# Kernel optimization log

Hardware: AMD Instinct MI355X
Metric: run time of the kernel (lower is better)

## Reference

```python
import jax, jax.numpy as jnp
import numpy as np

STRIDES = (8.0, 16.0, 32.0)


def _decode_level(feat, W, b, stride, level):
    # feat: [bs, C, ny, nx]; W: [85, C]; b: [85]
    bs, _, ny, nx = feat.shape
    # 1x1 conv == channel contraction; output laid out as [bs, ny, nx, 85]
    p = jnp.einsum('bchw,oc->bhwo', feat, W) + b
    y = jax.nn.sigmoid(p)
    xv = jnp.arange(nx, dtype=y.dtype)            # broadcasts over last spatial dim
    yv = jnp.arange(ny, dtype=y.dtype)[:, None]   # broadcasts over row dim
    power = jnp.asarray(2.0 ** level, dtype=y.dtype)
    d = (y[..., :4] * 2.0) ** 2 * power           # dx1, dy1, dx2, dy2
    x1 = (xv + 1.0 - d[..., 0]) * stride
    y1 = (yv + 1.0 - d[..., 1]) * stride
    x2 = (xv + d[..., 2]) * stride
    y2 = (yv + d[..., 3]) * stride
    # xyxy -> xywh
    box = jnp.stack([(x1 + x2) * 0.5, (y1 + y2) * 0.5, x2 - x1, y2 - y1], axis=-1)
    out = jnp.concatenate([box, y[..., 4:]], axis=-1)  # [bs, ny, nx, 85]
    return out.reshape(bs, ny * nx, out.shape[-1])


def setup_inputs() -> dict:
    key = jax.random.key(0)
    ks = jax.random.split(key, 9)
    f32 = jnp.float32
    return {
        'x0': jax.random.normal(ks[0], (16, 256, 80, 80), dtype=f32),
        'x1': jax.random.normal(ks[1], (16, 512, 40, 40), dtype=f32),
        'x2': jax.random.normal(ks[2], (16, 1024, 20, 20), dtype=f32),
        'W0': jax.random.normal(ks[3], (85, 256), dtype=f32) * 0.05,
        'b0': jax.random.normal(ks[4], (85,), dtype=f32) * 0.05,
        'W1': jax.random.normal(ks[5], (85, 512), dtype=f32) * 0.05,
        'b1': jax.random.normal(ks[6], (85,), dtype=f32) * 0.05,
        'W2': jax.random.normal(ks[7], (85, 1024), dtype=f32) * 0.05,
        'b2': jax.random.normal(ks[8], (85,), dtype=f32) * 0.05,
    }


def reference(x0, x1, x2, W0, b0, W1, b1, W2, b2):
    feats = (x0, x1, x2)
    Ws = (W0, W1, W2)
    bs_ = (b0, b1, b2)
    z = [_decode_level(feats[i], Ws[i], bs_[i], STRIDES[i], i) for i in range(3)]
    return jnp.concatenate(z, axis=1)  # [bs, 8400, 85]
```

## Files before the change

### kernel.cpp

```cpp
#include <hip/hip_runtime.h>
#include <cstdint>


typedef __attribute__((ext_vector_type(8))) short bf16x8;
typedef __attribute__((ext_vector_type(4))) float f32x4;

constexpr int KS0 = 8, KS1 = 16, KS2 = 32;
constexpr int F0 = 6 * KS0, F1 = 6 * KS1, F2 = 6 * KS2;
constexpr int FOFF0 = 0, FOFF1 = F0, FOFF2 = F0 + F1;
constexpr int NFRAG = F0 + F1 + F2;
constexpr size_t BIAS_OFF = 0;
constexpr size_t BPK_OFF  = 1152;
constexpr size_t WS_NEED  = BPK_OFF + (size_t)NFRAG * 64 * 16;

__device__ __forceinline__ unsigned short f2bf(float f) {
    union { float f; unsigned u; } v; v.f = f;
    unsigned r = v.u + 0x7FFF + ((v.u >> 16) & 1);
    return (unsigned short)(r >> 16);
}

__global__ __launch_bounds__(256) void prep_pack(
    const float* __restrict__ W0, const float* __restrict__ W1,
    const float* __restrict__ W2,
    const float* __restrict__ b0, const float* __restrict__ b1,
    const float* __restrict__ b2,
    unsigned char* __restrict__ ws)
{
    int t = blockIdx.x * 256 + threadIdx.x;
    if (t < 288) {
        int lvl = t / 96, o = t % 96;
        const float* bp = (lvl == 0) ? b0 : (lvl == 1) ? b1 : b2;
        ((float*)(ws + BIAS_OFF))[t] = (o < 85) ? bp[o] : 0.0f;
    }
    if (t >= NFRAG * 64) return;
    int frag = t >> 6, l = t & 63;
    int C; const float* W; int f;
    if (frag < FOFF1)      { C = 256;  W = W0; f = frag;         }
    else if (frag < FOFF2) { C = 512;  W = W1; f = frag - FOFF1; }
    else                   { C = 1024; W = W2; f = frag - FOFF2; }
    int ks = f / 6, n = f % 6;
    int o  = n * 16 + (l & 15);
    int c0 = ks * 32 + (l >> 4) * 8;
    bf16x8 r;
#pragma unroll
    for (int e = 0; e < 8; ++e)
        r[e] = (o < 85) ? (short)f2bf(W[(size_t)o * C + c0 + e]) : (short)0;
    ((bf16x8*)(ws + BPK_OFF))[frag * 64 + l] = r;
}

template <int C, int HW, int NX, int LEVEL, int AOFF, int KSTEPS, int FOFF>
__device__ __forceinline__ void mfma_level(
    const float* __restrict__ feat, const unsigned char* __restrict__ ws,
    float* __restrict__ out, int blk, uint4* __restrict__ Bsm )
{
    const int tid = threadIdx.x;
    const int w   = tid >> 6;
    const int l   = tid & 63;
    const int col = l & 15;
    const int kg  = l >> 4;
    const bool lo_half = (tid < 128);

    const int p0  = blk * 64 + w * 16;
    const int b   = p0 / HW;
    const int hw0 = p0 - b * HW;
    const float* fb = feat + (size_t)b * C * HW + hw0;
    const float* pA = fb + col + (size_t)(kg * 8) * HW;

    const float* bias = (const float*)(ws + BIAS_OFF) + LEVEL * 96;
    const uint4* bsrc = (const uint4*)(ws + BPK_OFF) + (size_t)FOFF * 64;

    f32x4 acc[6];
#pragma unroll
    for (int n = 0; n < 6; ++n) {
        float bv = bias[n * 16 + col];
        f32x4 z = { bv, bv, bv, bv };
        acc[n] = z;
    }

    uint4* buf0 = Bsm;
    uint4* buf1 = Bsm + 384;

    {
        const uint4* s = bsrc;
        buf0[tid] = s[tid];
        if (lo_half) buf0[256 + tid] = s[256 + tid];
    }
    float flA0[8], flA1[8];
#pragma unroll
    for (int e = 0; e < 8; ++e) flA0[e] = pA[(size_t)e * HW];
    if (KSTEPS > 1) {
        const float* p = pA + (size_t)32 * HW;
#pragma unroll
        for (int e = 0; e < 8; ++e) flA1[e] = p[(size_t)e * HW];
    }
    uint4 pb0, pb1;
    if (KSTEPS > 1) {
        const uint4* s = bsrc + 384;
        pb0 = s[tid];
        if (lo_half) pb1 = s[256 + tid];
    }
    __syncthreads();

#pragma unroll 1
    for (int ks = 0; ks < KSTEPS; ks += 2) {
        if (ks + 1 < KSTEPS) {
            buf1[tid] = pb0;
            if (lo_half) buf1[256 + tid] = pb1;
        }
        if (ks + 2 < KSTEPS) {
            const uint4* s = bsrc + (size_t)(ks + 2) * 384;
            pb0 = s[tid];
            if (lo_half) pb1 = s[256 + tid];
        }
        {
            bf16x8 a;
#pragma unroll
            for (int e = 0; e < 8; ++e) a[e] = (short)f2bf(flA0[e]);
            if (ks + 2 < KSTEPS) {
                const float* p = pA + (size_t)((ks + 2) * 32) * HW;
#pragma unroll
                for (int e = 0; e < 8; ++e) flA0[e] = p[(size_t)e * HW];
            }
            const bf16x8* bl = (const bf16x8*)buf0;
#pragma unroll
            for (int n = 0; n < 6; ++n) {
                bf16x8 bq = bl[n * 64 + l];
                acc[n] = __builtin_amdgcn_mfma_f32_16x16x32_bf16(a, bq, acc[n], 0, 0, 0);
            }
        }
        __syncthreads();

        if (ks + 2 < KSTEPS) {
            buf0[tid] = pb0;
            if (lo_half) buf0[256 + tid] = pb1;
        }
        if (ks + 3 < KSTEPS) {
            const uint4* s = bsrc + (size_t)(ks + 3) * 384;
            pb0 = s[tid];
            if (lo_half) pb1 = s[256 + tid];
        }
        if (ks + 1 < KSTEPS) {
            bf16x8 a;
#pragma unroll
            for (int e = 0; e < 8; ++e) a[e] = (short)f2bf(flA1[e]);
            if (ks + 3 < KSTEPS) {
                const float* p = pA + (size_t)((ks + 3) * 32) * HW;
#pragma unroll
                for (int e = 0; e < 8; ++e) flA1[e] = p[(size_t)e * HW];
            }
            const bf16x8* bl = (const bf16x8*)buf1;
#pragma unroll
            for (int n = 0; n < 6; ++n) {
                bf16x8 bq = bl[n * 64 + l];
                acc[n] = __builtin_amdgcn_mfma_f32_16x16x32_bf16(a, bq, acc[n], 0, 0, 0);
            }
        }
        __syncthreads();
    }

    constexpr float S  = (float)(8 << LEVEL);
    constexpr float P4 = 4.0f * (float)(1 << LEVEL);
#pragma unroll
    for (int j = 0; j < 4; ++j) {
        const int hw = hw0 + kg * 4 + j;
        float sg[6];
#pragma unroll
        for (int n = 0; n < 6; ++n) {
            float v = acc[n][j];
            sg[n] = __builtin_amdgcn_rcpf(1.0f + __expf(-v));
        }
        const int grp = l & 48;
        float y0 = __shfl(sg[0], grp + 0);
        float y1 = __shfl(sg[0], grp + 1);
        float y2 = __shfl(sg[0], grp + 2);
        float y3 = __shfl(sg[0], grp + 3);
        float wx = (float)(hw % NX);
        float wy = (float)(hw / NX);
        float d0 = y0 * y0 * P4, d1 = y1 * y1 * P4;
        float d2 = y2 * y2 * P4, d3 = y3 * y3 * P4;
        float x1 = (wx + 1.0f - d0) * S;
        float yA = (wy + 1.0f - d1) * S;
        float x2 = (wx + d2) * S;
        float yB = (wy + d3) * S;
        float bx = (x1 + x2) * 0.5f, by = (yA + yB) * 0.5f;
        float bw = x2 - x1,          bh = yB - yA;
        sg[0] = (col == 0) ? bx : (col == 1) ? by
              : (col == 2) ? bw : (col == 3) ? bh : sg[0];
        float* op = out + ((size_t)b * 8400 + AOFF + hw) * 85;
#pragma unroll
        for (int n = 0; n < 6; ++n) {
            int o = n * 16 + col;
            if (o < 85) op[o] = sg[n];
        }
    }
}

__global__ __launch_bounds__(256, 6) void detect_mfma(
    const float* __restrict__ x0, const float* __restrict__ x1,
    const float* __restrict__ x2,
    const unsigned char* __restrict__ ws, float* __restrict__ out)
{
    __shared__ uint4 Bsm[2 * 384];
    int blk = blockIdx.x;
    if (blk < 100)      mfma_level<1024, 400,  20, 2, 8000, KS2, FOFF2>(x2, ws, out, blk,       Bsm);
    else if (blk < 500) mfma_level<512,  1600, 40, 1, 6400, KS1, FOFF1>(x1, ws, out, blk - 100, Bsm);
    else                mfma_level<256,  6400, 80, 0, 0,    KS0, FOFF0>(x0, ws, out, blk - 500, Bsm);
}

template <int C, int HW, int NX, int LEVEL, int ONUM, bool BOX>
__device__ __forceinline__ void decode_path_fb(
    const float* __restrict__ feat, const float* __restrict__ Wm,
    const float* __restrict__ bias, float* __restrict__ out,
    int o_lo_in, int pos)
{
    const int o_lo = __builtin_amdgcn_readfirstlane(o_lo_in);
    const int b  = pos / HW;
    const int hw = pos - b * HW;
    const float* fp = feat + (size_t)b * (C * HW) + hw;
    float acc[ONUM];
#pragma unroll
    for (int j = 0; j < ONUM; ++j) acc[j] = bias[o_lo + j];
#pragma unroll 4
    for (int c = 0; c < C; ++c) {
        float fv = fp[(size_t)c * HW];
#pragma unroll
        for (int j = 0; j < ONUM; ++j)
            acc[j] = fmaf(fv, Wm[(o_lo + j) * C + c], acc[j]);
    }
#pragma unroll
    for (int j = 0; j < ONUM; ++j)
        acc[j] = __builtin_amdgcn_rcpf(1.0f + __expf(-acc[j]));
    constexpr float S = (float)(8 << LEVEL);
    constexpr int AOFF = (LEVEL == 0) ? 0 : ((LEVEL == 1) ? 6400 : 8000);
    float* op = out + ((size_t)b * 8400 + AOFF + hw) * 85 + o_lo;
    if constexpr (BOX) {
        constexpr float P4 = 4.0f * (float)(1 << LEVEL);
        float wx = (float)(hw % NX), wy = (float)(hw / NX);
        float d0 = acc[0] * acc[0] * P4, d1 = acc[1] * acc[1] * P4;
        float d2 = acc[2] * acc[2] * P4, d3 = acc[3] * acc[3] * P4;
        float x1 = (wx + 1.0f - d0) * S, y1 = (wy + 1.0f - d1) * S;
        float x2 = (wx + d2) * S,        y2 = (wy + d3) * S;
        op[0] = (x1 + x2) * 0.5f; op[1] = (y1 + y2) * 0.5f;
        op[2] = x2 - x1;          op[3] = y2 - y1;
#pragma unroll
        for (int j = 4; j < ONUM; ++j) op[j] = acc[j];
    } else {
#pragma unroll
        for (int j = 0; j < ONUM; ++j) op[j] = acc[j];
    }
}

template <int C, int HW, int NX, int LEVEL>
__device__ __forceinline__ void level_block_fb(
    const float* __restrict__ feat, const float* __restrict__ Wm,
    const float* __restrict__ bias, float* __restrict__ out, int bb)
{
    const int wave = threadIdx.x >> 6, lane = threadIdx.x & 63;
    const int pos = bb * 64 + lane;
    if      (wave == 0) decode_path_fb<C, HW, NX, LEVEL, 22, true >(feat, Wm, bias, out, 0,  pos);
    else if (wave == 1) decode_path_fb<C, HW, NX, LEVEL, 22, false>(feat, Wm, bias, out, 22, pos);
    else if (wave == 2) decode_path_fb<C, HW, NX, LEVEL, 22, false>(feat, Wm, bias, out, 44, pos);
    else                decode_path_fb<C, HW, NX, LEVEL, 19, false>(feat, Wm, bias, out, 66, pos);
}

__global__ __launch_bounds__(256) void detect_fallback(
    const float* __restrict__ x0, const float* __restrict__ x1,
    const float* __restrict__ x2,
    const float* __restrict__ w0, const float* __restrict__ w1,
    const float* __restrict__ w2,
    const float* __restrict__ b0, const float* __restrict__ b1,
    const float* __restrict__ b2, float* __restrict__ out)
{
    const int blk = blockIdx.x;
    if (blk < 100)      level_block_fb<1024, 400,  20, 2>(x2, w2, b2, out, blk);
    else if (blk < 500) level_block_fb<512,  1600, 40, 1>(x1, w1, b1, out, blk - 100);
    else                level_block_fb<256,  6400, 80, 0>(x0, w0, b0, out, blk - 500);
}

extern "C" void kernel_launch(void* const* d_in, const int* in_sizes, int n_in,
                              void* d_out, int out_size, void* d_ws, size_t ws_size,
                              hipStream_t stream)
{
    const float* x0 = (const float*)d_in[0];
    const float* x1 = (const float*)d_in[1];
    const float* x2 = (const float*)d_in[2];
    const float* W0 = (const float*)d_in[3];
    const float* b0 = (const float*)d_in[4];
    const float* W1 = (const float*)d_in[5];
    const float* b1 = (const float*)d_in[6];
    const float* W2 = (const float*)d_in[7];
    const float* b2 = (const float*)d_in[8];
    float* out = (float*)d_out;

    if (ws_size >= WS_NEED) {
        unsigned char* ws = (unsigned char*)d_ws;
        prep_pack<<<(NFRAG * 64 + 255) / 256, 256, 0, stream>>>(W0, W1, W2, b0, b1, b2, ws);
        detect_mfma<<<2100, 256, 0, stream>>>(x0, x1, x2, ws, out);
    } else {
        detect_fallback<<<2100, 256, 0, stream>>>(x0, x1, x2, W0, W1, W2, b0, b1, b2, out);
    }
}
```

Measured before the change: 48.35 us.

## Load packed weight fragments directly from global per wave, drop LDS staging and barriers

Removes the shared-memory double buffer for the packed B (weight) fragments and the block-wide __syncthreads. Each wave now reads its six bf16x8 weight fragments straight from global memory (expected to hit in L2/L1 since all waves share them) into registers, prefetching the next k-step's fragments after issuing the MFMAs. This removes barrier stalls and LDS traffic, letting waves progress independently, but adds redundant global loads per wave and more register pressure.

```diff
diff --git a/kernel.cpp b/kernel.cpp
--- a/kernel.cpp
+++ b/kernel.cpp
@@ -51,23 +51,20 @@
 template <int C, int HW, int NX, int LEVEL, int AOFF, int KSTEPS, int FOFF>
 __device__ __forceinline__ void mfma_level(
     const float* __restrict__ feat, const unsigned char* __restrict__ ws,
-    float* __restrict__ out, int blk, uint4* __restrict__ Bsm )
-{
-    const int tid = threadIdx.x;
-    const int w   = tid >> 6;
-    const int l   = tid & 63;
+    float* __restrict__ out, int subtile)
+{
+    const int l   = threadIdx.x & 63;
     const int col = l & 15;
     const int kg  = l >> 4;
-    const bool lo_half = (tid < 128);
-
-    const int p0  = blk * 64 + w * 16;
+
+    const int p0  = subtile * 16;
     const int b   = p0 / HW;
     const int hw0 = p0 - b * HW;
     const float* fb = feat + (size_t)b * C * HW + hw0;
     const float* pA = fb + col + (size_t)(kg * 8) * HW;
 
-    const float* bias = (const float*)(ws + BIAS_OFF) + LEVEL * 96;
-    const uint4* bsrc = (const uint4*)(ws + BPK_OFF) + (size_t)FOFF * 64;
+    const float*  bias = (const float*)(ws + BIAS_OFF) + LEVEL * 96;
+    const bf16x8* bp   = (const bf16x8*)(ws + BPK_OFF) + ((size_t)FOFF * 64 + l);
 
     f32x4 acc[6];
 #pragma unroll
@@ -77,41 +74,20 @@
         acc[n] = z;
     }
 
-    uint4* buf0 = Bsm;
-    uint4* buf1 = Bsm + 384;
-
+    float flA0[8], flA1[8];
+#pragma unroll
+    for (int e = 0; e < 8; ++e) flA0[e] = pA[(size_t)e * HW];
     {
-        const uint4* s = bsrc;
-        buf0[tid] = s[tid];
-        if (lo_half) buf0[256 + tid] = s[256 + tid];
-    }
-    float flA0[8], flA1[8];
-#pragma unroll
-    for (int e = 0; e < 8; ++e) flA0[e] = pA[(size_t)e * HW];
-    if (KSTEPS > 1) {
         const float* p = pA + (size_t)32 * HW;
 #pragma unroll
         for (int e = 0; e < 8; ++e) flA1[e] = p[(size_t)e * HW];
     }
-    uint4 pb0, pb1;
-    if (KSTEPS > 1) {
-        const uint4* s = bsrc + 384;
-        pb0 = s[tid];
-        if (lo_half) pb1 = s[256 + tid];
-    }
-    __syncthreads();
+    bf16x8 bq[6];
+#pragma unroll
+    for (int n = 0; n < 6; ++n) bq[n] = bp[(size_t)n * 64];
 
 #pragma unroll 1
     for (int ks = 0; ks < KSTEPS; ks += 2) {
-        if (ks + 1 < KSTEPS) {
-            buf1[tid] = pb0;
-            if (lo_half) buf1[256 + tid] = pb1;
-        }
-        if (ks + 2 < KSTEPS) {
-            const uint4* s = bsrc + (size_t)(ks + 2) * 384;
-            pb0 = s[tid];
-            if (lo_half) pb1 = s[256 + tid];
-        }
         {
             bf16x8 a;
 #pragma unroll
@@ -121,25 +97,14 @@
 #pragma unroll
                 for (int e = 0; e < 8; ++e) flA0[e] = p[(size_t)e * HW];
             }
-            const bf16x8* bl = (const bf16x8*)buf0;
-#pragma unroll
-            for (int n = 0; n < 6; ++n) {
-                bf16x8 bq = bl[n * 64 + l];
-                acc[n] = __builtin_amdgcn_mfma_f32_16x16x32_bf16(a, bq, acc[n], 0, 0, 0);
-            }
-        }
-        __syncthreads();
-
-        if (ks + 2 < KSTEPS) {
-            buf0[tid] = pb0;
-            if (lo_half) buf0[256 + tid] = pb1;
-        }
-        if (ks + 3 < KSTEPS) {
-            const uint4* s = bsrc + (size_t)(ks + 3) * 384;
-            pb0 = s[tid];
-            if (lo_half) pb1 = s[256 + tid];
-        }
-        if (ks + 1 < KSTEPS) {
+#pragma unroll
+            for (int n = 0; n < 6; ++n)
+                acc[n] = __builtin_amdgcn_mfma_f32_16x16x32_bf16(a, bq[n], acc[n], 0, 0, 0);
+#pragma unroll
+            for (int n = 0; n < 6; ++n)
+                bq[n] = bp[((size_t)(ks + 1) * 6 + n) * 64];
+        }
+        {
             bf16x8 a;
 #pragma unroll
             for (int e = 0; e < 8; ++e) a[e] = (short)f2bf(flA1[e]);
@@ -148,14 +113,15 @@
 #pragma unroll
                 for (int e = 0; e < 8; ++e) flA1[e] = p[(size_t)e * HW];
             }
-            const bf16x8* bl = (const bf16x8*)buf1;
-#pragma unroll
-            for (int n = 0; n < 6; ++n) {
-                bf16x8 bq = bl[n * 64 + l];
-                acc[n] = __builtin_amdgcn_mfma_f32_16x16x32_bf16(a, bq, acc[n], 0, 0, 0);
+#pragma unroll
+            for (int n = 0; n < 6; ++n)
+                acc[n] = __builtin_amdgcn_mfma_f32_16x16x32_bf16(a, bq[n], acc[n], 0, 0, 0);
+            if (ks + 2 < KSTEPS) {
+#pragma unroll
+                for (int n = 0; n < 6; ++n)
+                    bq[n] = bp[((size_t)(ks + 2) * 6 + n) * 64];
             }
         }
-        __syncthreads();
     }
 
     constexpr float S  = (float)(8 << LEVEL);
@@ -200,11 +166,14 @@
     const float* __restrict__ x2,
     const unsigned char* __restrict__ ws, float* __restrict__ out)
 {
-    __shared__ uint4 Bsm[2 * 384];
-    int blk = blockIdx.x;
-    if (blk < 100)      mfma_level<1024, 400,  20, 2, 8000, KS2, FOFF2>(x2, ws, out, blk,       Bsm);
-    else if (blk < 500) mfma_level<512,  1600, 40, 1, 6400, KS1, FOFF1>(x1, ws, out, blk - 100, Bsm);
-    else                mfma_level<256,  6400, 80, 0, 0,    KS0, FOFF0>(x0, ws, out, blk - 500, Bsm);
+    const int blk = blockIdx.x;
+    const int w   = threadIdx.x >> 6;
+    if (blk < 100)
+        mfma_level<1024, 400,  20, 2, 8000, KS2, FOFF2>(x2, ws, out, blk * 4 + w);
+    else if (blk < 500)
+        mfma_level<512,  1600, 40, 1, 6400, KS1, FOFF1>(x1, ws, out, (blk - 100) * 4 + w);
+    else
+        mfma_level<256,  6400, 80, 0, 0,    KS0, FOFF0>(x0, ws, out, (blk - 500) * 4 + w);
 }
 
 template <int C, int HW, int NX, int LEVEL, int ONUM, bool BOX>
```

Measured after the change: 85.19 us. +76.2%, slower.
